# Performance work log

Hardware: AMD Instinct MI355X
Metric: run time of the kernel (lower is better)

Reference implementation:

```python
import jax, jax.numpy as jnp
import numpy as np

B, T, C = 4, 2048, 2048
EPS = 1e-5


def setup_inputs() -> dict:
    key = jax.random.key(0)
    ks = jax.random.split(key, 9)
    s = 1.0 / np.sqrt(C)
    return {
        "x": jax.random.normal(ks[0], (B, T, C), jnp.float32),
        "ln_w": jnp.ones((C,), jnp.float32),
        "ln_b": jnp.zeros((C,), jnp.float32),
        "mix_k": jax.random.uniform(ks[1], (C,), jnp.float32),
        "mix_v": jax.random.uniform(ks[2], (C,), jnp.float32),
        "mix_r": jax.random.uniform(ks[3], (C,), jnp.float32),
        "time_decay": jnp.zeros((C,), jnp.float32),
        "time_first": jnp.zeros((C,), jnp.float32),
        "Wk": jax.random.normal(ks[4], (C, C), jnp.float32) * s,
        "Wv": jax.random.normal(ks[5], (C, C), jnp.float32) * s,
        "Wr": jax.random.normal(ks[6], (C, C), jnp.float32) * s,
        "Wo": jax.random.normal(ks[7], (C, C), jnp.float32) * s,
    }


def reference(x, ln_w, ln_b, mix_k, mix_v, mix_r, time_decay, time_first, Wk, Wv, Wr, Wo):
    # LayerNorm over channel dim
    mu = jnp.mean(x, axis=-1, keepdims=True)
    var = jnp.var(x, axis=-1, keepdims=True)
    xt = (x - mu) * jax.lax.rsqrt(var + EPS) * ln_w + ln_b  # [B,T,C]

    # x_prev at step t is xt at step t-1 (zeros at t=0) -> simple time shift
    prev = jnp.concatenate([jnp.zeros_like(xt[:, :1]), xt[:, :-1]], axis=1)

    # Batched projections (torch Linear: y = x @ W.T)
    k = jnp.einsum('btc,dc->btd', xt * mix_k + prev * (1.0 - mix_k), Wk)
    v = jnp.einsum('btc,dc->btd', xt * mix_v + prev * (1.0 - mix_v), Wv)
    r = jax.nn.sigmoid(jnp.einsum('btc,dc->btd', xt * mix_r + prev * (1.0 - mix_r), Wr))

    decay = jax.nn.sigmoid(time_decay)  # [C]
    first = jnp.exp(time_first)         # [C]

    # Elementwise linear recurrence: state_t = decay * state_{t-1} + k_t
    def step(state, k_t):
        state = state * decay + k_t
        return state, state

    _, states = jax.lax.scan(step, jnp.zeros((B, C), x.dtype), jnp.swapaxes(k, 0, 1))
    state = jnp.swapaxes(states, 0, 1)  # [B,T,C]

    rwkv = (state * first + k) * v
    return jnp.einsum('btc,dc->btd', r * rwkv, Wo)
```

## Files before the change

### kernel.cpp

```cpp
#include <hip/hip_runtime.h>
#include <math.h>

constexpr int B_ = 4;
constexpr int T_ = 2048;
constexpr int C_ = 2048;
constexpr int M_ = B_ * T_;
constexpr float EPS_ = 1e-5f;
constexpr int KSTEPS = C_ / 64;
constexpr int NCH = 32;
constexpr int CHL = T_ / NCH;

typedef __attribute__((ext_vector_type(8))) short short8;
typedef __attribute__((ext_vector_type(4))) float f32x4;

__device__ __forceinline__ unsigned short rne_bf16(float x) {
    unsigned u = __float_as_uint(x);
    unsigned r = u + 0x7FFFu + ((u >> 16) & 1u);
    return (unsigned short)(r >> 16);
}

__global__ __launch_bounds__(256) void ln_mix3_kernel(
        const float* __restrict__ x,
        const float* __restrict__ w,
        const float* __restrict__ bias,
        const float* __restrict__ mxk,
        const float* __restrict__ mxv,
        const float* __restrict__ mxr,
        unsigned short* __restrict__ ak,
        unsigned short* __restrict__ av,
        unsigned short* __restrict__ ar) {
    const int m = blockIdx.x;
    const int tid = threadIdx.x;
    const bool hasPrev = (m & (T_ - 1)) != 0;
    const float* xm = x + (size_t)m * C_;

    float4 a0 = ((const float4*)xm)[tid];
    float4 a1 = ((const float4*)xm)[tid + 256];
    float4 p0 = make_float4(0.f, 0.f, 0.f, 0.f), p1 = p0;
    if (hasPrev) {
        p0 = ((const float4*)(xm - C_))[tid];
        p1 = ((const float4*)(xm - C_))[tid + 256];
    }

    float sm = a0.x + a0.y + a0.z + a0.w + a1.x + a1.y + a1.z + a1.w;
    float qm = a0.x*a0.x + a0.y*a0.y + a0.z*a0.z + a0.w*a0.w
             + a1.x*a1.x + a1.y*a1.y + a1.z*a1.z + a1.w*a1.w;
    float sp = p0.x + p0.y + p0.z + p0.w + p1.x + p1.y + p1.z + p1.w;
    float qp = p0.x*p0.x + p0.y*p0.y + p0.z*p0.z + p0.w*p0.w
             + p1.x*p1.x + p1.y*p1.y + p1.z*p1.z + p1.w*p1.w;

    #pragma unroll
    for (int off = 32; off > 0; off >>= 1) {
        sm += __shfl_down(sm, off, 64);
        qm += __shfl_down(qm, off, 64);
        sp += __shfl_down(sp, off, 64);
        qp += __shfl_down(qp, off, 64);
    }
    __shared__ float red[20];
    const int wid = tid >> 6, lane = tid & 63;
    if (lane == 0) {
        red[wid * 4 + 0] = sm; red[wid * 4 + 1] = qm;
        red[wid * 4 + 2] = sp; red[wid * 4 + 3] = qp;
    }
    __syncthreads();
    if (tid == 0) {
        float tsm = 0.f, tqm = 0.f, tsp = 0.f, tqp = 0.f;
        #pragma unroll
        for (int i = 0; i < 4; ++i) {
            tsm += red[i * 4 + 0]; tqm += red[i * 4 + 1];
            tsp += red[i * 4 + 2]; tqp += red[i * 4 + 3];
        }
        const float mum = tsm / (float)C_;
        const float varm = tqm / (float)C_ - mum * mum;
        const float mup = tsp / (float)C_;
        const float varp = tqp / (float)C_ - mup * mup;
        red[16] = mum; red[17] = rsqrtf(varm + EPS_);
        red[18] = mup; red[19] = rsqrtf(varp + EPS_);
    }
    __syncthreads();
    const float mum = red[16], rsm = red[17];
    const float mup = red[18], rsp = red[19];

    float4 w0 = ((const float4*)w)[tid];
    float4 w1 = ((const float4*)w)[tid + 256];
    float4 b0 = ((const float4*)bias)[tid];
    float4 b1 = ((const float4*)bias)[tid + 256];

    const float avv[8] = {a0.x, a0.y, a0.z, a0.w, a1.x, a1.y, a1.z, a1.w};
    const float pvv[8] = {p0.x, p0.y, p0.z, p0.w, p1.x, p1.y, p1.z, p1.w};
    const float wvv[8] = {w0.x, w0.y, w0.z, w0.w, w1.x, w1.y, w1.z, w1.w};
    const float bvv[8] = {b0.x, b0.y, b0.z, b0.w, b1.x, b1.y, b1.z, b1.w};

    float lm[8], lp[8];
    #pragma unroll
    for (int j = 0; j < 8; ++j) {
        lm[j] = (avv[j] - mum) * rsm * wvv[j] + bvv[j];
        lp[j] = hasPrev ? (pvv[j] - mup) * rsp * wvv[j] + bvv[j] : 0.f;
    }

    const size_t rowbase = (size_t)m * C_;
    auto emit = [&](const float* __restrict__ mx, unsigned short* __restrict__ hi) {
        float4 m0 = ((const float4*)mx)[tid];
        float4 m1 = ((const float4*)mx)[tid + 256];
        const float mm[8] = {m0.x, m0.y, m0.z, m0.w, m1.x, m1.y, m1.z, m1.w};
        ushort4 h[2];
        #pragma unroll
        for (int half = 0; half < 2; ++half) {
            unsigned short hh[4];
            #pragma unroll
            for (int j = 0; j < 4; ++j) {
                const int c = half * 4 + j;
                hh[j] = rne_bf16(lp[c] + (lm[c] - lp[c]) * mm[c]);
            }
            h[half].x = hh[0]; h[half].y = hh[1]; h[half].z = hh[2]; h[half].w = hh[3];
        }
        ((ushort4*)(hi + rowbase))[tid] = h[0];
        ((ushort4*)(hi + rowbase))[tid + 256] = h[1];
    };
    emit(mxk, ak);
    emit(mxv, av);
    emit(mxr, ar);
}

__global__ __launch_bounds__(256) void wconv_kernel(const float* __restrict__ W,
                                                    unsigned short* __restrict__ hi) {
    const int i = blockIdx.x * 256 + threadIdx.x;
    float4 w = ((const float4*)W)[i];
    ushort4 h;
    h.x = rne_bf16(w.x);
    h.y = rne_bf16(w.y);
    h.z = rne_bf16(w.z);
    h.w = rne_bf16(w.w);
    ((ushort4*)hi)[i] = h;
}

template <bool SIG>
__global__ __launch_bounds__(512, 2) void gemm_mfma(const unsigned short* __restrict__ Ahi,
                                                    const unsigned short* __restrict__ Whi,
                                                    float* __restrict__ Y) {
    __shared__ unsigned short lds[2][2][256 * 64];

    const int tid = threadIdx.x;
    const int lane = tid & 63;
    const int wid = tid >> 6;
    const int wr = wid >> 2;
    const int wcn = wid & 3;

    const int bid = blockIdx.x;
    const int swz = (bid & 7) * 32 + (bid >> 3);
    const int m0 = (swz >> 3) * 256;
    const int n0 = (swz & 7) * 256;

    const unsigned short* gA[4];
    const unsigned short* gB[4];
    #pragma unroll
    for (int j = 0; j < 4; ++j) {
        const int ci = j * 512 + tid;
        const int r = ci >> 3, p = ci & 7;
        const int s = p ^ (r & 7);
        gA[j] = Ahi + (size_t)(m0 + r) * C_ + s * 8;
        gB[j] = Whi + (size_t)(n0 + r) * C_ + s * 8;
    }
    const int stage_off = wid * 512;

    const int fr = lane & 15;
    const int kg = lane >> 4;
    const int pS0 = (kg + 0) ^ (fr & 7);
    const int pS1 = (kg + 4) ^ (fr & 7);
    const int baseA0 = (wr * 128 + fr) * 64 + pS0 * 8;
    const int baseA1 = (wr * 128 + fr) * 64 + pS1 * 8;
    const int baseB0 = (wcn * 64 + fr) * 64 + pS0 * 8;
    const int baseB1 = (wcn * 64 + fr) * 64 + pS1 * 8;

    f32x4 acc[8][4] = {};

    auto ISSUE = [&](int buf, int t, int j) {
        const int ko = t * 64;
        __builtin_amdgcn_global_load_lds(
            (const __attribute__((address_space(1))) unsigned int*)(gA[j] + ko),
            (__attribute__((address_space(3))) unsigned int*)&lds[buf][0][j * 4096 + stage_off],
            16, 0, 0);
        __builtin_amdgcn_global_load_lds(
            (const __attribute__((address_space(1))) unsigned int*)(gB[j] + ko),
            (__attribute__((address_space(3))) unsigned int*)&lds[buf][1][j * 4096 + stage_off],
            16, 0, 0);
    };

    auto MFMA_PAIR = [&](int mi0, const short8& a0s0, const short8& a0s1,
                         const short8& a1s0, const short8& a1s1,
                         const short8* b0, const short8* b1) {
        #pragma unroll
        for (int ni = 0; ni < 4; ++ni) {
            acc[mi0][ni]     = __builtin_amdgcn_mfma_f32_16x16x32_bf16(a0s0, b0[ni], acc[mi0][ni], 0, 0, 0);
            acc[mi0 + 1][ni] = __builtin_amdgcn_mfma_f32_16x16x32_bf16(a1s0, b0[ni], acc[mi0 + 1][ni], 0, 0, 0);
        }
        #pragma unroll
        for (int ni = 0; ni < 4; ++ni) {
            acc[mi0][ni]     = __builtin_amdgcn_mfma_f32_16x16x32_bf16(a0s1, b1[ni], acc[mi0][ni], 0, 0, 0);
            acc[mi0 + 1][ni] = __builtin_amdgcn_mfma_f32_16x16x32_bf16(a1s1, b1[ni], acc[mi0 + 1][ni], 0, 0, 0);
        }
    };

    #pragma unroll
    for (int j = 0; j < 4; ++j) ISSUE(0, 0, j);

    for (int t = 0; t < KSTEPS; ++t) {
        const int cur = t & 1, nxt = cur ^ 1;
        const bool last = (t == KSTEPS - 1);
        const unsigned short* LA = lds[cur][0];
        const unsigned short* LB = lds[cur][1];

        short8 b0[4], b1[4];

        if (!last) {
            ISSUE(nxt, t + 1, 0);
            asm volatile("s_waitcnt vmcnt(2)" ::: "memory");
        } else {
            asm volatile("s_waitcnt vmcnt(0)" ::: "memory");
        }
        __builtin_amdgcn_s_barrier();
        #pragma unroll
        for (int ni = 0; ni < 4; ++ni) {
            b0[ni] = *(const short8*)&LB[baseB0 + ni * 1024];
            b1[ni] = *(const short8*)&LB[baseB1 + ni * 1024];
        }
        {
            const short8 a0s0 = *(const short8*)&LA[baseA0 + 0 * 1024];
            const short8 a0s1 = *(const short8*)&LA[baseA1 + 0 * 1024];
            const short8 a1s0 = *(const short8*)&LA[baseA0 + 1 * 1024];
            const short8 a1s1 = *(const short8*)&LA[baseA1 + 1 * 1024];
            asm volatile("s_waitcnt lgkmcnt(0)" ::: "memory");
            __builtin_amdgcn_s_setprio(1);
            MFMA_PAIR(0, a0s0, a0s1, a1s0, a1s1, b0, b1);
            __builtin_amdgcn_s_setprio(0);
        }
        __builtin_amdgcn_s_barrier();

        #pragma unroll
        for (int p = 1; p < 4; ++p) {
            const int mi0 = 2 * p;
            const short8 a0s0 = *(const short8*)&LA[baseA0 + mi0 * 1024];
            const short8 a0s1 = *(const short8*)&LA[baseA1 + mi0 * 1024];
            const short8 a1s0 = *(const short8*)&LA[baseA0 + (mi0 + 1) * 1024];
            const short8 a1s1 = *(const short8*)&LA[baseA1 + (mi0 + 1) * 1024];
            if (!last) ISSUE(nxt, t + 1, p);
            __builtin_amdgcn_s_barrier();
            asm volatile("s_waitcnt lgkmcnt(0)" ::: "memory");
            __builtin_amdgcn_s_setprio(1);
            MFMA_PAIR(mi0, a0s0, a0s1, a1s0, a1s1, b0, b1);
            __builtin_amdgcn_s_setprio(0);
            __builtin_amdgcn_s_barrier();
        }
    }

    const int orow = m0 + wr * 128 + (lane >> 4) * 4;
    const int ocol = n0 + wcn * 64 + fr;
    #pragma unroll
    for (int mi = 0; mi < 8; ++mi)
        #pragma unroll
        for (int ni = 0; ni < 4; ++ni)
            #pragma unroll
            for (int rr = 0; rr < 4; ++rr) {
                float v = acc[mi][ni][rr];
                if (SIG) v = 1.f / (1.f + expf(-v));
                Y[(size_t)(orow + mi * 16 + rr) * C_ + ocol + ni * 16] = v;
            }
}

__global__ __launch_bounds__(256) void wkv_scan1(const float* __restrict__ k,
                                                 const float* __restrict__ time_decay,
                                                 float* __restrict__ chend) {
    const int c0 = (blockIdx.x * 256 + threadIdx.x) * 2;
    const int j = blockIdx.y;
    const int b = blockIdx.z;
    const float2 td = *(const float2*)&time_decay[c0];
    const float d0 = 1.f / (1.f + expf(-td.x));
    const float d1 = 1.f / (1.f + expf(-td.y));
    size_t base = ((size_t)b * T_ + (size_t)j * CHL) * C_ + c0;
    float s0 = 0.f, s1 = 0.f;
    #pragma unroll 8
    for (int t = 0; t < CHL; ++t) {
        const float2 kt = *(const float2*)&k[base];
        s0 = s0 * d0 + kt.x;
        s1 = s1 * d1 + kt.y;
        base += C_;
    }
    *(float2*)&chend[((size_t)b * NCH + j) * C_ + c0] = make_float2(s0, s1);
}

__global__ __launch_bounds__(256) void wkv_scan2(const float* __restrict__ k,
                                                 const float* __restrict__ v,
                                                 const float* __restrict__ r,
                                                 const float* __restrict__ time_decay,
                                                 const float* __restrict__ time_first,
                                                 const float* __restrict__ chend,
                                                 unsigned short* __restrict__ yhi) {
    const int c0 = (blockIdx.x * 256 + threadIdx.x) * 2;
    const int j = blockIdx.y;
    const int b = blockIdx.z;
    const float2 td = *(const float2*)&time_decay[c0];
    const float2 tf = *(const float2*)&time_first[c0];
    const float d0 = 1.f / (1.f + expf(-td.x));
    const float d1 = 1.f / (1.f + expf(-td.y));
    const float f0 = expf(tf.x);
    const float f1 = expf(tf.y);

    float dL0 = d0, dL1 = d1;
    #pragma unroll
    for (int i = 0; i < 6; ++i) { dL0 *= dL0; dL1 *= dL1; }

    float s0 = 0.f, s1 = 0.f;
    for (int i = 0; i < j; ++i) {
        const float2 e = *(const float2*)&chend[((size_t)b * NCH + i) * C_ + c0];
        s0 = s0 * dL0 + e.x;
        s1 = s1 * dL1 + e.y;
    }

    size_t base = ((size_t)b * T_ + (size_t)j * CHL) * C_ + c0;
    #pragma unroll 4
    for (int t = 0; t < CHL; ++t) {
        const float2 kt = *(const float2*)&k[base];
        const float2 vt = *(const float2*)&v[base];
        const float2 rt = *(const float2*)&r[base];
        s0 = s0 * d0 + kt.x;
        s1 = s1 * d1 + kt.y;
        const float y0 = rt.x * ((s0 * f0 + kt.x) * vt.x);
        const float y1 = rt.y * ((s1 * f1 + kt.y) * vt.y);
        ushort2 ph; ph.x = rne_bf16(y0); ph.y = rne_bf16(y1);
        *(ushort2*)&yhi[base] = ph;
        base += C_;
    }
}

extern "C" void kernel_launch(void* const* d_in, const int* in_sizes, int n_in,
                              void* d_out, int out_size, void* d_ws, size_t ws_size,
                              hipStream_t stream) {
    const float* x          = (const float*)d_in[0];
    const float* ln_w       = (const float*)d_in[1];
    const float* ln_b       = (const float*)d_in[2];
    const float* mix_k      = (const float*)d_in[3];
    const float* mix_v      = (const float*)d_in[4];
    const float* mix_r      = (const float*)d_in[5];
    const float* time_decay = (const float*)d_in[6];
    const float* time_first = (const float*)d_in[7];
    const float* Wk         = (const float*)d_in[8];
    const float* Wv         = (const float*)d_in[9];
    const float* Wr         = (const float*)d_in[10];
    const float* Wo         = (const float*)d_in[11];
    float* out = (float*)d_out;

    const size_t planeElems = (size_t)M_ * C_;
    unsigned short* akhi = (unsigned short*)d_ws;
    unsigned short* avhi = akhi + 2 * planeElems;
    unsigned short* arhi = avhi + 2 * planeElems;
    unsigned short* whi  = arhi + 2 * planeElems;

    float* kb = (float*)arhi;
    float* vb = (float*)akhi;
    float* rb = out;
    unsigned short* yhi = avhi;
    float* chend = (float*)whi;

    const int wcBlocks = (C_ * C_ / 4) / 256;
    const dim3 wkvGrid(C_ / 512, NCH, B_);

    ln_mix3_kernel<<<M_, 256, 0, stream>>>(x, ln_w, ln_b, mix_k, mix_v, mix_r,
                                           akhi, avhi, arhi);

    wconv_kernel<<<wcBlocks, 256, 0, stream>>>(Wr, whi);
    gemm_mfma<true><<<256, 512, 0, stream>>>(arhi, whi, rb);

    wconv_kernel<<<wcBlocks, 256, 0, stream>>>(Wk, whi);
    gemm_mfma<false><<<256, 512, 0, stream>>>(akhi, whi, kb);

    wconv_kernel<<<wcBlocks, 256, 0, stream>>>(Wv, whi);
    gemm_mfma<false><<<256, 512, 0, stream>>>(avhi, whi, vb);

    wkv_scan1<<<wkvGrid, 256, 0, stream>>>(kb, time_decay, chend);
    wkv_scan2<<<wkvGrid, 256, 0, stream>>>(kb, vb, rb, time_decay, time_first, chend,
                                           yhi);

    wconv_kernel<<<wcBlocks, 256, 0, stream>>>(Wo, whi);
    gemm_mfma<false><<<256, 512, 0, stream>>>(yhi, whi, out);
}
```

Measured before the change: 385.1 us.

## Shrink GEMM tile to 128x128 with 256-thread blocks and more blocks

Changes the bf16 MFMA GEMM from 256x256 tiles with 8 waves to 128x128 tiles with 4 waves, launching 1024 blocks instead of 256. The prefetch schedule now issues two load chunks per phase in two phases per k-step. This aims to improve load balance and latency hiding through more resident blocks. The cost is lower per-block data reuse and more global/L2 traffic.

```diff
diff --git a/kernel.cpp b/kernel.cpp
--- a/kernel.cpp
+++ b/kernel.cpp
@@ -135,27 +135,27 @@
 }
 
 template <bool SIG>
-__global__ __launch_bounds__(512, 2) void gemm_mfma(const unsigned short* __restrict__ Ahi,
+__global__ __launch_bounds__(256, 2) void gemm_mfma(const unsigned short* __restrict__ Ahi,
                                                     const unsigned short* __restrict__ Whi,
                                                     float* __restrict__ Y) {
-    __shared__ unsigned short lds[2][2][256 * 64];
+    __shared__ unsigned short lds[2][2][128 * 64];
 
     const int tid = threadIdx.x;
     const int lane = tid & 63;
     const int wid = tid >> 6;
-    const int wr = wid >> 2;
-    const int wcn = wid & 3;
+    const int wr = wid >> 1;
+    const int wc = wid & 1;
 
     const int bid = blockIdx.x;
-    const int swz = (bid & 7) * 32 + (bid >> 3);
-    const int m0 = (swz >> 3) * 256;
-    const int n0 = (swz & 7) * 256;
+    const int swz = (bid & 7) * 128 + (bid >> 3);
+    const int m0 = (swz >> 4) * 128;
+    const int n0 = (swz & 15) * 128;
 
     const unsigned short* gA[4];
     const unsigned short* gB[4];
     #pragma unroll
     for (int j = 0; j < 4; ++j) {
-        const int ci = j * 512 + tid;
+        const int ci = j * 256 + tid;
         const int r = ci >> 3, p = ci & 7;
         const int s = p ^ (r & 7);
         gA[j] = Ahi + (size_t)(m0 + r) * C_ + s * 8;
@@ -167,22 +167,22 @@
     const int kg = lane >> 4;
     const int pS0 = (kg + 0) ^ (fr & 7);
     const int pS1 = (kg + 4) ^ (fr & 7);
-    const int baseA0 = (wr * 128 + fr) * 64 + pS0 * 8;
-    const int baseA1 = (wr * 128 + fr) * 64 + pS1 * 8;
-    const int baseB0 = (wcn * 64 + fr) * 64 + pS0 * 8;
-    const int baseB1 = (wcn * 64 + fr) * 64 + pS1 * 8;
-
-    f32x4 acc[8][4] = {};
+    const int baseA0 = (wr * 64 + fr) * 64 + pS0 * 8;
+    const int baseA1 = (wr * 64 + fr) * 64 + pS1 * 8;
+    const int baseB0 = (wc * 64 + fr) * 64 + pS0 * 8;
+    const int baseB1 = (wc * 64 + fr) * 64 + pS1 * 8;
+
+    f32x4 acc[4][4] = {};
 
     auto ISSUE = [&](int buf, int t, int j) {
         const int ko = t * 64;
         __builtin_amdgcn_global_load_lds(
             (const __attribute__((address_space(1))) unsigned int*)(gA[j] + ko),
-            (__attribute__((address_space(3))) unsigned int*)&lds[buf][0][j * 4096 + stage_off],
+            (__attribute__((address_space(3))) unsigned int*)&lds[buf][0][j * 2048 + stage_off],
             16, 0, 0);
         __builtin_amdgcn_global_load_lds(
             (const __attribute__((address_space(1))) unsigned int*)(gB[j] + ko),
-            (__attribute__((address_space(3))) unsigned int*)&lds[buf][1][j * 4096 + stage_off],
+            (__attribute__((address_space(3))) unsigned int*)&lds[buf][1][j * 2048 + stage_off],
             16, 0, 0);
     };
 
@@ -214,7 +214,8 @@
 
         if (!last) {
             ISSUE(nxt, t + 1, 0);
-            asm volatile("s_waitcnt vmcnt(2)" ::: "memory");
+            ISSUE(nxt, t + 1, 1);
+            asm volatile("s_waitcnt vmcnt(4)" ::: "memory");
         } else {
             asm volatile("s_waitcnt vmcnt(0)" ::: "memory");
         }
@@ -236,27 +237,28 @@
         }
         __builtin_amdgcn_s_barrier();
 
-        #pragma unroll
-        for (int p = 1; p < 4; ++p) {
-            const int mi0 = 2 * p;
-            const short8 a0s0 = *(const short8*)&LA[baseA0 + mi0 * 1024];
-            const short8 a0s1 = *(const short8*)&LA[baseA1 + mi0 * 1024];
-            const short8 a1s0 = *(const short8*)&LA[baseA0 + (mi0 + 1) * 1024];
-            const short8 a1s1 = *(const short8*)&LA[baseA1 + (mi0 + 1) * 1024];
-            if (!last) ISSUE(nxt, t + 1, p);
+        {
+            const short8 a0s0 = *(const short8*)&LA[baseA0 + 2 * 1024];
+            const short8 a0s1 = *(const short8*)&LA[baseA1 + 2 * 1024];
+            const short8 a1s0 = *(const short8*)&LA[baseA0 + 3 * 1024];
+            const short8 a1s1 = *(const short8*)&LA[baseA1 + 3 * 1024];
+            if (!last) {
+                ISSUE(nxt, t + 1, 2);
+                ISSUE(nxt, t + 1, 3);
+            }
             __builtin_amdgcn_s_barrier();
             asm volatile("s_waitcnt lgkmcnt(0)" ::: "memory");
             __builtin_amdgcn_s_setprio(1);
-            MFMA_PAIR(mi0, a0s0, a0s1, a1s0, a1s1, b0, b1);
+            MFMA_PAIR(2, a0s0, a0s1, a1s0, a1s1, b0, b1);
             __builtin_amdgcn_s_setprio(0);
             __builtin_amdgcn_s_barrier();
         }
     }
 
-    const int orow = m0 + wr * 128 + (lane >> 4) * 4;
-    const int ocol = n0 + wcn * 64 + fr;
-    #pragma unroll
-    for (int mi = 0; mi < 8; ++mi)
+    const int orow = m0 + wr * 64 + (lane >> 4) * 4;
+    const int ocol = n0 + wc * 64 + fr;
+    #pragma unroll
+    for (int mi = 0; mi < 4; ++mi)
         #pragma unroll
         for (int ni = 0; ni < 4; ++ni)
             #pragma unroll
@@ -362,24 +364,25 @@
     float* chend = (float*)whi;
 
     const int wcBlocks = (C_ * C_ / 4) / 256;
+    const int gemmBlocks = (M_ / 128) * (C_ / 128);
     const dim3 wkvGrid(C_ / 512, NCH, B_);
 
     ln_mix3_kernel<<<M_, 256, 0, stream>>>(x, ln_w, ln_b, mix_k, mix_v, mix_r,
                                            akhi, avhi, arhi);
 
     wconv_kernel<<<wcBlocks, 256, 0, stream>>>(Wr, whi);
-    gemm_mfma<true><<<256, 512, 0, stream>>>(arhi, whi, rb);
+    gemm_mfma<true><<<gemmBlocks, 256, 0, stream>>>(arhi, whi, rb);
 
     wconv_kernel<<<wcBlocks, 256, 0, stream>>>(Wk, whi);
-    gemm_mfma<false><<<256, 512, 0, stream>>>(akhi, whi, kb);
+    gemm_mfma<false><<<gemmBlocks, 256, 0, stream>>>(akhi, whi, kb);
 
     wconv_kernel<<<wcBlocks, 256, 0, stream>>>(Wv, whi);
-    gemm_mfma<false><<<256, 512, 0, stream>>>(avhi, whi, vb);
+    gemm_mfma<false><<<gemmBlocks, 256, 0, stream>>>(avhi, whi, vb);
 
     wkv_scan1<<<wkvGrid, 256, 0, stream>>>(kb, time_decay, chend);
     wkv_scan2<<<wkvGrid, 256, 0, stream>>>(kb, vb, rb, time_decay, time_first, chend,
                                            yhi);
 
     wconv_kernel<<<wcBlocks, 256, 0, stream>>>(Wo, whi);
-    gemm_mfma<false><<<256, 512, 0, stream>>>(yhi, whi, out);
-}
+    gemm_mfma<false><<<gemmBlocks, 256, 0, stream>>>(yhi, whi, out);
+}
```

Result: slower. 436.7 us (+13.4%).
